# Optimization experiments

Hardware: AMD Instinct MI355X
Metric: run time of the kernel (lower is better)

The kernel has to match this reference:

```python
import jax, jax.numpy as jnp
from jax import lax
import numpy as np

V, T, K, R, H, EN, L = 10000, 100, 50, 300, 200, 800, 3
B = 128
TRAIN_SIZE = 100000
DELTA = 0.005


def setup_inputs():
    key = jax.random.key(0)
    ks = jax.random.split(key, 16)
    s = 0.02
    return {
        "bows": jax.random.uniform(ks[0], (B, V), jnp.float32) * 10.0 + 1e-3,
        "times": jax.random.randint(ks[1], (B,), 0, T),
        "rnn_inp": jax.random.uniform(ks[2], (T, V), jnp.float32),
        "rho_W": jax.random.normal(ks[3], (V, R), jnp.float32) * s,
        "mu_q_alpha": jax.random.normal(ks[4], (K, T, R), jnp.float32),
        "logsigma_q_alpha": jax.random.normal(ks[5], (K, T, R), jnp.float32) * 0.1 - 2.0,
        "qtheta_W1": jax.random.normal(ks[6], (EN, V + K), jnp.float32) * s,
        "qtheta_b1": jnp.zeros((EN,), jnp.float32),
        "qtheta_W2": jax.random.normal(ks[7], (EN, EN), jnp.float32) * s,
        "qtheta_b2": jnp.zeros((EN,), jnp.float32),
        "mu_theta_W": jax.random.normal(ks[8], (K, EN), jnp.float32) * s,
        "mu_theta_b": jnp.zeros((K,), jnp.float32),
        "ls_theta_W": jax.random.normal(ks[9], (K, EN), jnp.float32) * s,
        "ls_theta_b": jnp.zeros((K,), jnp.float32),
        "eta_map_W": jax.random.normal(ks[10], (H, V), jnp.float32) * s,
        "eta_map_b": jnp.zeros((H,), jnp.float32),
        "lstm_Wih": jax.random.normal(ks[11], (L, 4 * H, H), jnp.float32) * s,
        "lstm_Whh": jax.random.normal(ks[12], (L, 4 * H, H), jnp.float32) * s,
        "lstm_bih": jnp.zeros((L, 4 * H), jnp.float32),
        "lstm_bhh": jnp.zeros((L, 4 * H), jnp.float32),
        "mu_eta_W": jax.random.normal(ks[13], (K, H + K), jnp.float32) * s,
        "mu_eta_b": jnp.zeros((K,), jnp.float32),
        "ls_eta_W": jax.random.normal(ks[14], (K, H + K), jnp.float32) * s,
        "ls_eta_b": jnp.zeros((K,), jnp.float32),
    }


def _kl(q_mu, q_ls, p_mu, p_ls):
    # KL(N(q_mu, exp(q_ls)) || N(p_mu, exp(p_ls))), logsigma == log-variance as in torch code
    return 0.5 * jnp.sum((jnp.exp(q_ls) + (q_mu - p_mu) ** 2) / (jnp.exp(p_ls) + 1e-6) - 1.0 + p_ls - q_ls, axis=-1)


def _lstm(x, Wih, Whh, bih, bhh):
    # x: [T, H]; L stacked LSTM layers (batch of 1 squeezed), torch gate order i,f,g,o
    for l in range(Wih.shape[0]):
        Wi, Wh, bi, bh = Wih[l], Whh[l], bih[l], bhh[l]
        Hd = Wh.shape[1]

        def step(carry, xt, Wi=Wi, Wh=Wh, bi=bi, bh=bh):
            h, c = carry
            g = Wi @ xt + Wh @ h + bi + bh
            i, f, gg, o = jnp.split(g, 4)
            c = jax.nn.sigmoid(f) * c + jax.nn.sigmoid(i) * jnp.tanh(gg)
            h = jax.nn.sigmoid(o) * jnp.tanh(c)
            return (h, c), h

        z = jnp.zeros((Hd,), x.dtype)
        _, x = lax.scan(step, (z, z), x)
    return x


def _forward(bows, rnn_inp, rho_W, mu_q_alpha, logsigma_q_alpha, qtheta_W1, qtheta_b1, qtheta_W2, qtheta_b2, mu_theta_W, mu_theta_b, ls_theta_W, ls_theta_b, eta_map_W, eta_map_b, lstm_Wih, lstm_Whh, lstm_bih, lstm_bhh, mu_eta_W, mu_eta_b, ls_eta_W, ls_eta_b, times):
    log_delta = jnp.log(jnp.float32(DELTA))
    # --- eta: LSTM over word-freq sequence, then sequential mu/logsigma/KL per t ---
    out = _lstm(rnn_inp @ eta_map_W.T + eta_map_b, lstm_Wih, lstm_Whh, lstm_bih, lstm_bhh)  # [T,H]
    p_ls_seq = jnp.concatenate([jnp.zeros((1,), jnp.float32), jnp.full((T - 1,), log_delta, jnp.float32)])

    def eta_step(eta_prev, xs):
        o_t, p_ls = xs
        x = jnp.concatenate([o_t, eta_prev])
        mu = mu_eta_W @ x + mu_eta_b
        ls = ls_eta_W @ x + ls_eta_b
        kl = _kl(mu, ls, eta_prev, jnp.full_like(mu, p_ls))
        return mu, (mu, kl)  # eval-mode reparameterize -> eta_t = mu

    _, (etas, kls) = lax.scan(eta_step, jnp.zeros((K,), jnp.float32), (out, p_ls_seq))
    kl_eta = kls.sum()
    # --- theta encoder ---
    nb = bows / bows.sum(1, keepdims=True)
    eta_td = etas[times]  # [B,K]
    h = jax.nn.relu(jnp.concatenate([nb, eta_td], axis=1) @ qtheta_W1.T + qtheta_b1)
    h = jax.nn.relu(h @ qtheta_W2.T + qtheta_b2)
    mu_t = h @ mu_theta_W.T + mu_theta_b
    ls_t = h @ ls_theta_W.T + ls_theta_b
    theta = jax.nn.softmax(mu_t, axis=-1)  # z = mu (eval-mode reparam)
    coeff = jnp.float32(TRAIN_SIZE / bows.shape[0])
    kl_theta = _kl(mu_t, ls_t, eta_td, jnp.zeros_like(mu_t)).sum() * coeff
    # --- alpha: with eval-mode reparam, alphas == mu, so KL is fully vectorized ---
    muT = jnp.transpose(mu_q_alpha, (1, 0, 2))  # [T,K,R]
    lsT = jnp.transpose(logsigma_q_alpha, (1, 0, 2))
    alphas = muT
    p_mu = jnp.concatenate([jnp.zeros((1, K, R), muT.dtype), alphas[:-1]], axis=0)
    p_ls = jnp.concatenate([jnp.zeros((1, K, R), muT.dtype), jnp.full((T - 1, K, R), log_delta, muT.dtype)], axis=0)
    kl_alpha = _kl(muT, lsT, p_mu, p_ls).sum()
    # --- beta and NLL ---
    logit = alphas.reshape(T * K, R) @ rho_W.T  # [T*K, V]
    beta = jax.nn.softmax(logit, axis=-1).reshape(T, K, V)
    beta_d = beta[times]  # [B,K,V]
    loglik = jnp.log(jnp.einsum('bk,bkv->bv', theta, beta_d) + 1e-12)
    nll = (-(loglik * bows).sum(-1)).sum() * coeff
    loss = nll + kl_eta + kl_theta + kl_alpha
    return loss, nll, kl_eta, kl_theta, kl_alpha


def reference(bows, times, rnn_inp, rho_W, mu_q_alpha, logsigma_q_alpha, qtheta_W1, qtheta_b1, qtheta_W2, qtheta_b2, mu_theta_W, mu_theta_b, ls_theta_W, ls_theta_b, eta_map_W, eta_map_b, lstm_Wih, lstm_Whh, lstm_bih, lstm_bhh, mu_eta_W, mu_eta_b, ls_eta_W, ls_eta_b):
    return _forward(bows, rnn_inp, rho_W, mu_q_alpha, logsigma_q_alpha, qtheta_W1, qtheta_b1, qtheta_W2, qtheta_b2, mu_theta_W, mu_theta_b, ls_theta_W, ls_theta_b, eta_map_W, eta_map_b, lstm_Wih, lstm_Whh, lstm_bih, lstm_bhh, mu_eta_W, mu_eta_b, ls_eta_W, ls_eta_b, times)
```

## Files before the change

kernel.cpp:

```cpp
#include <hip/hip_runtime.h>


typedef unsigned int u32;
typedef unsigned short u16;
typedef _Float16 f16;
typedef f16 f16x2 __attribute__((ext_vector_type(2)));
typedef short bf16x8 __attribute__((ext_vector_type(8)));
typedef float f32x4 __attribute__((ext_vector_type(4)));
typedef u32 u32x4 __attribute__((ext_vector_type(4)));

#define LOG_DELTA (-5.2983174f)
#define COEFF 781.25f

#if defined(__has_builtin)
#if __has_builtin(__builtin_amdgcn_sdot4)
#define HAVE_SDOT4 1
#endif
#endif

__device__ __forceinline__ float bf2f(u16 a) { return __uint_as_float(((u32)a) << 16); }
__device__ __forceinline__ u16 f2bf(float f) {
  u32 u = __float_as_uint(f);
  u32 r = (u + 0x7fffu + ((u >> 16) & 1u)) >> 16;
  return (u16)r;
}
__device__ __forceinline__ float fdot2(u32 w, u32 h, float acc) {
  return __builtin_amdgcn_fdot2(__builtin_bit_cast(f16x2, w), __builtin_bit_cast(f16x2, h), acc, false);
}
__device__ __forceinline__ int dot4i8(u32 a, u32 b, int c) {
#ifdef HAVE_SDOT4
  return __builtin_amdgcn_sdot4(a, b, c, false);
#else
  int s = c;
  s += ((int)(a << 24) >> 24) * ((int)(b << 24) >> 24);
  s += ((int)(a << 16) >> 24) * ((int)(b << 16) >> 24);
  s += ((int)(a << 8) >> 24) * ((int)(b << 8) >> 24);
  s += ((int)a >> 24) * ((int)b >> 24);
  return s;
#endif
}
__device__ __forceinline__ float sigm(float x) { return 1.f / (1.f + __expf(-x)); }
__device__ __forceinline__ float ftanh(float x) { float t = __expf(2.f * x); return (t - 1.f) / (t + 1.f); }
__device__ __forceinline__ u16 f2h(float x) { return __builtin_bit_cast(u16, (f16)x); }
__device__ __forceinline__ float h2f(u16 x) { return (float)__builtin_bit_cast(f16, x); }
__device__ __forceinline__ void async_load16(const u16* g, u16* l) {
  __builtin_amdgcn_global_load_lds((const __attribute__((address_space(1))) u32*)g,
                                   (__attribute__((address_space(3))) u32*)l, 16, 0, 0);
}


__global__ __launch_bounds__(64) void k_zero(float* __restrict__ accum) {
  if (threadIdx.x < 8) accum[threadIdx.x] = 0.f;
}

__global__ __launch_bounds__(256) void k_nb(const float* __restrict__ bows, float* __restrict__ nb) {
  __shared__ float red[256];
  const int b = blockIdx.x, tid = threadIdx.x;
  float s = 0.f;
  for (int v = tid; v < 10000; v += 256) s += bows[b * 10000 + v];
  red[tid] = s; __syncthreads();
  for (int o = 128; o > 0; o >>= 1) { if (tid < o) red[tid] += red[tid + o]; __syncthreads(); }
  const float inv = 1.f / red[0];
  for (int v = tid; v < 10000; v += 256) nb[b * 10000 + v] = bows[b * 10000 + v] * inv;
}

__global__ __launch_bounds__(256) void k_bsum(const float* __restrict__ a, const float* __restrict__ b,
                                              float* __restrict__ o, int n) {
  int i = blockIdx.x * 256 + threadIdx.x;
  if (i < n) o[i] = a[i] + b[i];
}

__global__ __launch_bounds__(256) void k_fill(float* __restrict__ C, const float* __restrict__ bias,
                                              int N, int total) {
  for (int i = blockIdx.x * 256 + threadIdx.x; i < total; i += gridDim.x * 256)
    C[i] = bias[i % N];
}

__global__ __launch_bounds__(256) void k_relu(float* __restrict__ C, int total) {
  for (int i = blockIdx.x * 256 + threadIdx.x; i < total; i += gridDim.x * 256) {
    float v = C[i];
    C[i] = v > 0.f ? v : 0.f;
  }
}

__global__ __launch_bounds__(128) void k_stack2(const float* __restrict__ a, const float* __restrict__ b,
                                                float* __restrict__ o) {
  const int t = threadIdx.x;
  if (t < 50) o[t] = a[t];
  else if (t < 100) o[t] = b[t - 50];
}

__global__ __launch_bounds__(64) void k_quant_whh(const float* __restrict__ Whh,
                                                  u32* __restrict__ whq, float* __restrict__ rowscale) {
  const int gr = blockIdx.x;
  const int lane = threadIdx.x;
  __shared__ float wrow[200];
  const float* src = Whh + (size_t)gr * 200;
  float m = 0.f;
  for (int c = lane; c < 200; c += 64) { float v = src[c]; wrow[c] = v; m = fmaxf(m, fabsf(v)); }
  for (int o = 32; o > 0; o >>= 1) m = fmaxf(m, __shfl_down(m, o));
  m = __shfl(m, 0);
  const float qs = (m > 0.f) ? 127.f / m : 0.f;
  __syncthreads();
  const int l = gr / 800, rr = gr - l * 800;
  if (lane < 52) {
    u32 d = 0;
    if (lane < 50) {
#pragma unroll
      for (int b = 0; b < 4; ++b) {
        int q = __float2int_rn(wrow[lane * 4 + b] * qs);
        q = max(-127, min(127, q));
        d |= ((u32)(q & 0xff)) << (8 * b);
      }
    }
    whq[l * 41600 + rr * 52 + lane] = d;
  }
  if (lane == 0) rowscale[gr] = (m > 0.f) ? m / 127.f : 0.f;
}

__global__ __launch_bounds__(256) void k_cvt_eta(const float* __restrict__ muW, const float* __restrict__ lsW,
                                                 u16* __restrict__ out) {
  int idx = blockIdx.x * 256 + threadIdx.x;
  if (idx >= 25000) return;
  int r = idx / 250, c = idx - r * 250;
  float v = (r < 50) ? muW[r * 250 + c] : lsW[(r - 50) * 250 + c];
  out[idx] = f2h(v);
}

__global__ __launch_bounds__(256) void k_prep_A(const float* __restrict__ muq, u16* __restrict__ Abf) {
  int idx = blockIdx.x * 256 + threadIdx.x;
  if (idx >= 5120 * 320) return;
  int r = idx % 320, m = idx / 320;
  float v = 0.f;
  if (r < 300 && m < 5000) { int t = m / 50, k = m - t * 50; v = muq[k * 30000 + t * 300 + r]; }
  Abf[idx] = f2bf(v);
}
__global__ __launch_bounds__(256) void k_prep_B(const float* __restrict__ rho, u16* __restrict__ Bbf) {
  int idx = blockIdx.x * 256 + threadIdx.x;
  if (idx >= 10112 * 320) return;
  int r = idx % 320, n = idx / 320;
  float v = (r < 300 && n < 10000) ? rho[n * 300 + r] : 0.f;
  Bbf[idx] = f2bf(v);
}


#define ST 64
#define SBK 32

template<int AMODE, int BMODE, int EPI>
__global__ __launch_bounds__(256) void gemm64(
    const float* __restrict__ A, const float* __restrict__ Bm, const float* __restrict__ Bm2,
    const float* __restrict__ bias, float* __restrict__ C,
    int M, int N, int Kd, int lda, int ldb,
    const int* __restrict__ times, const float* __restrict__ etas)
{
  __shared__ __align__(16) float As[SBK][ST + 4];
  __shared__ __align__(16) float Bs[SBK][ST + 4];
  const int tid = threadIdx.x;
  const int tx = tid & 15, ty = tid >> 4;
  const int m_base = blockIdx.x * ST, n_base = blockIdx.y * ST;
  float acc[4][4] = {};
  const int nkt = (Kd + SBK - 1) / SBK;
  const int per = (nkt + gridDim.z - 1) / gridDim.z;
  const int kt0 = blockIdx.z * per;
  const int kt1 = min(nkt, kt0 + per);
  const int lkk = tid & 31;
  const int lrow = tid >> 5;
  for (int kt = kt0; kt < kt1; ++kt) {
    const int kg = kt * SBK + lkk;
#pragma unroll
    for (int i = 0; i < 8; ++i) {
      const int m = m_base + lrow + i * 8;
      float v = 0.f;
      if (m < M && kg < Kd) {
        if (AMODE == 0) v = A[(size_t)m * lda + kg];
        else {
          if (kg < 10000) v = A[(size_t)m * 10000 + kg];
          else v = etas[times[m] * 50 + (kg - 10000)];
        }
      }
      As[lkk][lrow + i * 8] = v;
    }
#pragma unroll
    for (int i = 0; i < 8; ++i) {
      const int n = n_base + lrow + i * 8;
      float v = 0.f;
      if (n < N && kg < Kd) {
        if (BMODE == 0) v = Bm[(size_t)n * ldb + kg];
        else v = (n < 50) ? Bm[(size_t)n * ldb + kg] : Bm2[(size_t)(n - 50) * ldb + kg];
      }
      Bs[lkk][lrow + i * 8] = v;
    }
    __syncthreads();
#pragma unroll
    for (int kk = 0; kk < SBK; ++kk) {
      const float4 a4 = *(const float4*)&As[kk][ty * 4];
      const float4 b4 = *(const float4*)&Bs[kk][tx * 4];
      const float av[4] = {a4.x, a4.y, a4.z, a4.w};
      const float bv[4] = {b4.x, b4.y, b4.z, b4.w};
#pragma unroll
      for (int i = 0; i < 4; ++i)
#pragma unroll
        for (int j = 0; j < 4; ++j) acc[i][j] += av[i] * bv[j];
    }
    __syncthreads();
  }
#pragma unroll
  for (int i = 0; i < 4; ++i) {
    const int m = m_base + ty * 4 + i;
    if (m >= M) continue;
#pragma unroll
    for (int j = 0; j < 4; ++j) {
      const int n = n_base + tx * 4 + j;
      if (n >= N) continue;
      float v = acc[i][j];
      if (EPI == 1) { C[(size_t)m * N + n] = v + bias[n]; }
      else if (EPI == 2) { v += bias[n]; C[(size_t)m * N + n] = v > 0.f ? v : 0.f; }
      else if (EPI == 5) { atomicAdd(&C[(size_t)m * N + n], v); }
      else { C[(size_t)m * N + n] = v; }
    }
  }
}


__global__ __launch_bounds__(256) void gemm_mfma_bT(
    const u16* __restrict__ A, const u16* __restrict__ B, u16* __restrict__ C,
    int M, int N)
{
  __shared__ u16 As[128 * 32];
  __shared__ u16 Bs[128 * 32];
  const int tid = threadIdx.x;
  const int l = tid & 63, w = tid >> 6;
  const int wm = w & 1, wn = w >> 1;
  const int m0 = blockIdx.x * 128, n0 = blockIdx.y * 128;
  f32x4 acc[4][4] = {};
  const int arow = l >> 2;
  const int acol = (l & 3) * 8;
  for (int kt = 0; kt < 10; ++kt) {
    const int k0 = kt * 32;
#pragma unroll
    for (int c = 0; c < 2; ++c) {
      const int i = w + c * 4;
      async_load16(A + (size_t)(m0 + i * 16 + arow) * 320 + k0 + acol, As + i * 512);
      async_load16(B + (size_t)(n0 + i * 16 + arow) * 320 + k0 + acol, Bs + i * 512);
    }
    __syncthreads();
    bf16x8 af[4], bfr[4];
#pragma unroll
    for (int x = 0; x < 4; ++x) {
      af[x]  = *(const bf16x8*)&As[(wm * 64 + x * 16 + (l & 15)) * 32 + (l >> 4) * 8];
      bfr[x] = *(const bf16x8*)&Bs[(wn * 64 + x * 16 + (l & 15)) * 32 + (l >> 4) * 8];
    }
#pragma unroll
    for (int x = 0; x < 4; ++x)
#pragma unroll
      for (int y = 0; y < 4; ++y)
        acc[x][y] = __builtin_amdgcn_mfma_f32_16x16x32_bf16(af[x], bfr[y], acc[x][y], 0, 0, 0);
    __syncthreads();
  }
  const int col = l & 15, quad = l >> 4;
#pragma unroll
  for (int x = 0; x < 4; ++x) {
    const int gmB = m0 + wm * 64 + x * 16 + quad * 4;
#pragma unroll
    for (int y = 0; y < 4; ++y) {
      const int gn = n0 + wn * 64 + y * 16 + col;
      if (gn >= N) continue;
#pragma unroll
      for (int r = 0; r < 4; ++r) {
        const int gm = gmB + r;
        if (gm < M) C[(size_t)gm * N + gn] = f2bf(acc[x][y][r]);
      }
    }
  }
}


__global__ __launch_bounds__(512, 1) void lstm_scan_reg(
    const u32* __restrict__ whq,
    const float* __restrict__ rowscale,
    const float* __restrict__ xproj,
    float* __restrict__ hseq,
    u16* __restrict__ hseq16,
    const int write16)
{
  __shared__ u16 pg[800];
  __shared__ __align__(16) u32 hq[52];
  __shared__ float wmax[8];
  __shared__ float hscale_s[1];
  const int tid = threadIdx.x;
  const int act = (tid < 400);
  const int r0 = tid, r1 = tid + 400;
  u32x4 wA4[13], wB4[13];
  float rsA = 0.f, rsB = 0.f;
  float xpA = 0.f, xpB = 0.f;
  if (act) {
    const u32x4* gA = (const u32x4*)(whq + (size_t)r0 * 52);
    const u32x4* gB = (const u32x4*)(whq + (size_t)r1 * 52);
#pragma unroll
    for (int i = 0; i < 13; ++i) { wA4[i] = gA[i]; wB4[i] = gB[i]; }
    rsA = rowscale[r0]; rsB = rowscale[r1];
    xpA = xproj[r0]; xpB = xproj[r1];
  }
  if (tid < 52) hq[tid] = 0;
  if (tid < 8) wmax[tid] = 0.f;
  if (tid == 0) hscale_s[0] = 0.f;
  float c_reg = 0.f;
  __syncthreads();
  for (int t = 0; t < 100; ++t) {
    if (act) {
      float nxA = 0.f, nxB = 0.f;
      if (t < 99) { nxA = xproj[(t + 1) * 800 + r0]; nxB = xproj[(t + 1) * 800 + r1]; }
      const float hdq = hscale_s[0];
      u32x4 hv4[13];
#pragma unroll
      for (int i = 0; i < 13; ++i) hv4[i] = *((const u32x4*)hq + i);
      int aA = 0, aB = 0;
#pragma unroll
      for (int g = 0; g < 50; ++g) {
        const u32 h = hv4[g >> 2][g & 3];
        aA = dot4i8(wA4[g >> 2][g & 3], h, aA);
        aB = dot4i8(wB4[g >> 2][g & 3], h, aB);
      }
      pg[r0] = f2h((float)aA * (rsA * hdq) + xpA);
      pg[r1] = f2h((float)aB * (rsB * hdq) + xpB);
      xpA = nxA; xpB = nxB;
    }
    __syncthreads();
    float hv = 0.f;
    if (tid < 200) {
      float gi = sigm(h2f(pg[tid]));
      float gf = sigm(h2f(pg[200 + tid]));
      float gg = ftanh(h2f(pg[400 + tid]));
      float go = sigm(h2f(pg[600 + tid]));
      c_reg = gf * c_reg + gi * gg;
      hv = go * ftanh(c_reg);
      hseq[t * 200 + tid] = hv;
      if (write16) hseq16[t * 200 + tid] = f2h(hv);
    }
    float m = fabsf(hv);
    for (int o = 32; o > 0; o >>= 1) m = fmaxf(m, __shfl_down(m, o));
    if ((tid & 63) == 0) wmax[tid >> 6] = m;
    __syncthreads();
    if (tid < 200) {
      const float hm = fmaxf(fmaxf(wmax[0], wmax[1]), fmaxf(wmax[2], wmax[3]));
      const float qs = (hm > 0.f) ? 127.f / hm : 0.f;
      int q = __float2int_rn(hv * qs);
      q = max(-127, min(127, q));
      ((signed char*)hq)[tid] = (signed char)q;
      if (tid == 0) hscale_s[0] = (hm > 0.f) ? hm / 127.f : 0.f;
    }
    __syncthreads();
  }
}


__global__ __launch_bounds__(512) void eta_scan(
    const u16* __restrict__ etaWh,
    const float* __restrict__ mub, const float* __restrict__ lsb,
    const u16* __restrict__ hseq16,
    float* __restrict__ etas, float* __restrict__ accum)
{
  __shared__ __align__(4) u16 EW[25000];
  __shared__ __align__(4) u16 HS[20000];
  __shared__ __align__(4) u16 xh[252];
  __shared__ float pc[400];
  __shared__ float mu_ls[100];
  __shared__ float bias[100];
  __shared__ float eta_f[52];
  const int tid = threadIdx.x;
  for (int i = tid; i < 12500; i += 512) ((u32*)EW)[i] = ((const u32*)etaWh)[i];
  for (int i = tid; i < 10000; i += 512) ((u32*)HS)[i] = ((const u32*)hseq16)[i];
  if (tid < 100) bias[tid] = (tid < 50) ? mub[tid] : lsb[tid - 50];
  if (tid < 52) eta_f[tid] = 0.f;
  if (tid < 252) xh[tid] = 0;
  float klacc = 0.f;
  const int r = tid % 100, s4 = tid / 100;
  const int q0 = s4 * 32, q1 = min(125, q0 + 32);
  __syncthreads();
  for (int t = 0; t < 100; ++t) {
    if (tid < 100) ((u32*)xh)[tid] = ((const u32*)HS)[t * 100 + tid];
    __syncthreads();
    if (tid < 400) {
      float acc = 0.f;
      const u32* Wr = (const u32*)EW;
      const u32* X2 = (const u32*)xh;
      for (int q = q0; q < q1; ++q) acc = fdot2(Wr[r * 125 + q], X2[q], acc);
      pc[s4 * 100 + r] = acc;
    }
    __syncthreads();
    if (tid < 100)
      mu_ls[tid] = pc[tid] + pc[100 + tid] + pc[200 + tid] + pc[300 + tid] + bias[tid];
    __syncthreads();
    if (tid < 50) {
      float mu = mu_ls[tid], ls = mu_ls[50 + tid], ep = eta_f[tid];
      float pls = (t == 0) ? 0.f : LOG_DELTA;
      float pv = __expf(pls) + 1e-6f;
      float d = mu - ep;
      klacc += 0.5f * ((__expf(ls) + d * d) / pv - 1.f + pls - ls);
      etas[t * 50 + tid] = mu;
      eta_f[tid] = mu;
      xh[200 + tid] = f2h(mu);
    }
    __syncthreads();
  }
  if (tid < 64) {
    for (int o = 32; o > 0; o >>= 1) klacc += __shfl_down(klacc, o);
    if (tid == 0) accum[0] = klacc;
  }
}


__global__ __launch_bounds__(64) void k_theta(const float* __restrict__ mul,
                                              const float* __restrict__ etas, const int* __restrict__ times,
                                              float* __restrict__ theta, float* __restrict__ accum) {
  const int b = blockIdx.x, lane = threadIdx.x;
  float m_ = 0.f, l_ = 0.f, e_ = 0.f, mx = -1e30f;
  if (lane < 50) {
    m_ = mul[b * 100 + lane];
    l_ = mul[b * 100 + 50 + lane];
    e_ = etas[times[b] * 50 + lane];
    mx = m_;
  }
  for (int o = 32; o > 0; o >>= 1) mx = fmaxf(mx, __shfl_down(mx, o));
  mx = __shfl(mx, 0);
  float ex = (lane < 50) ? __expf(m_ - mx) : 0.f;
  float sum = ex;
  for (int o = 32; o > 0; o >>= 1) sum += __shfl_down(sum, o);
  sum = __shfl(sum, 0);
  if (lane < 50) theta[b * 50 + lane] = ex / sum;
  float kl = 0.f;
  if (lane < 50) {
    float d = m_ - e_;
    kl = 0.5f * ((__expf(l_) + d * d) / (1.f + 1e-6f) - 1.f - l_);
  }
  for (int o = 32; o > 0; o >>= 1) kl += __shfl_down(kl, o);
  if (lane == 0) atomicAdd(accum + 1, kl);
}


__global__ __launch_bounds__(256) void k_rowsum(const u16* __restrict__ logit, float* __restrict__ Z) {
  const int r = blockIdx.x, tid = threadIdx.x;
  const u32* row = (const u32*)(logit + (size_t)r * 10000);
  __shared__ float red[256];
  float s = 0.f;
  for (int v = tid; v < 5000; v += 256) {
    u32 p = row[v];
    s += __expf(bf2f((u16)(p & 0xffffu))) + __expf(bf2f((u16)(p >> 16)));
  }
  red[tid] = s; __syncthreads();
  for (int o = 128; o > 0; o >>= 1) { if (tid < o) red[tid] += red[tid + o]; __syncthreads(); }
  if (tid == 0) Z[r] = red[0];
}


__global__ __launch_bounds__(256) void k_nll(const u16* __restrict__ logit, const float* __restrict__ Z,
                                             const float* __restrict__ theta, const float* __restrict__ bows,
                                             const int* __restrict__ times, float* __restrict__ accum) {
  const int b = blockIdx.x, seg = blockIdx.y, tid = threadIdx.x;
  const int t = times[b];
  __shared__ float c2[52];
  __shared__ float red[256];
  if (tid < 50) c2[tid] = theta[b * 50 + tid] / Z[t * 50 + tid];
  __syncthreads();
  float part = 0.f;
  const int v0 = seg * 1250, v1 = v0 + 1250;
  const u16* base = logit + (size_t)t * 500000;
  for (int v = v0 + tid; v < v1; v += 256) {
    float ssv = 1e-12f;
#pragma unroll
    for (int k = 0; k < 50; ++k) ssv += c2[k] * __expf(bf2f(base[k * 10000 + v]));
    part += bows[b * 10000 + v] * __logf(ssv);
  }
  red[tid] = part; __syncthreads();
  for (int o = 128; o > 0; o >>= 1) { if (tid < o) red[tid] += red[tid + o]; __syncthreads(); }
  if (tid == 0) atomicAdd(accum + 3, -red[0]);
}


__global__ __launch_bounds__(256) void k_alpha_kl(const float* __restrict__ muq, const float* __restrict__ lsq,
                                                  float* __restrict__ accum) {
  __shared__ float red[256];
  const int tid = threadIdx.x;
  float s = 0.f;
  for (int i = blockIdx.x * 256 + tid; i < 1500000; i += gridDim.x * 256) {
    int r = i % 300;
    int tk = i / 300;
    int k = tk % 50;
    int t = tk / 50;
    size_t idx = (size_t)k * 30000 + (size_t)t * 300 + r;
    float mu = muq[idx], ls = lsq[idx];
    float pm = 0.f, pls = 0.f;
    if (t > 0) { pm = muq[idx - 300]; pls = LOG_DELTA; }
    float d = mu - pm;
    s += 0.5f * ((__expf(ls) + d * d) / (__expf(pls) + 1e-6f) - 1.f + pls - ls);
  }
  red[tid] = s; __syncthreads();
  for (int o = 128; o > 0; o >>= 1) { if (tid < o) red[tid] += red[tid + o]; __syncthreads(); }
  if (tid == 0) atomicAdd(accum + 2, red[0]);
}


__global__ __launch_bounds__(64) void k_final(const float* __restrict__ accum, float* __restrict__ out) {
  if (threadIdx.x == 0) {
    float nll = accum[3] * COEFF;
    float kl_eta = accum[0];
    float kl_theta = accum[1] * COEFF;
    float kl_alpha = accum[2];
    out[0] = nll + kl_eta + kl_theta + kl_alpha;
    out[1] = nll;
    out[2] = kl_eta;
    out[3] = kl_theta;
    out[4] = kl_alpha;
  }
}


extern "C" void kernel_launch(void* const* d_in, const int* in_sizes, int n_in,
                              void* d_out, int out_size, void* d_ws, size_t ws_size,
                              hipStream_t stream) {
  (void)in_sizes; (void)n_in; (void)out_size; (void)ws_size;
  const float* bows   = (const float*)d_in[0];
  const int*   times  = (const int*)d_in[1];
  const float* rnn_in = (const float*)d_in[2];
  const float* rho_W  = (const float*)d_in[3];
  const float* muq    = (const float*)d_in[4];
  const float* lsq    = (const float*)d_in[5];
  const float* qW1    = (const float*)d_in[6];
  const float* qb1    = (const float*)d_in[7];
  const float* qW2    = (const float*)d_in[8];
  const float* qb2    = (const float*)d_in[9];
  const float* muthW  = (const float*)d_in[10];
  const float* muthb  = (const float*)d_in[11];
  const float* lsthW  = (const float*)d_in[12];
  const float* lsthb  = (const float*)d_in[13];
  const float* emW    = (const float*)d_in[14];
  const float* emb    = (const float*)d_in[15];
  const float* Wih    = (const float*)d_in[16];
  const float* Whh    = (const float*)d_in[17];
  const float* bih    = (const float*)d_in[18];
  const float* bhh    = (const float*)d_in[19];
  const float* mueW   = (const float*)d_in[20];
  const float* mueb   = (const float*)d_in[21];
  const float* lseW   = (const float*)d_in[22];
  const float* lseb   = (const float*)d_in[23];
  float* out = (float*)d_out;
  float* ws = (float*)d_ws;

  float* accum = ws + 0;
  float* nb    = ws + 8;
  float* x0    = ws + 1280008;
  float* xproj = ws + 1300008;
  float* hsA   = ws + 1380008;
  float* hsB   = ws + 1400008;
  u32*   whq   = (u32*)(ws + 1420008);
  float* rowsc = ws + 1544808;
  float* bias2 = ws + 1547208;
  u16*   etaWh = (u16*)(ws + 1547408);
  float* hsC   = ws + 1560008;
  u16*   hs16  = (u16*)(ws + 1580008);
  float* bsum  = ws + 1660008;
  float* etas  = ws + 1662408;
  float* h1    = ws + 1667408;
  float* h2    = ws + 1769808;
  float* mul   = ws + 1872208;
  float* theta = ws + 1885008;
  float* Zrow  = ws + 1891408;
  u16*   A_bf  = (u16*)(ws + 1896408);
  u16*   B_bf  = (u16*)(ws + 2715608);
  u16*   logit = (u16*)(ws + 4333528);

  k_zero<<<1, 64, 0, stream>>>(accum);
  k_nb<<<128, 256, 0, stream>>>(bows, nb);
  k_quant_whh<<<2400, 64, 0, stream>>>(Whh, whq, rowsc);
  k_bsum<<<10, 256, 0, stream>>>(bih, bhh, bsum, 2400);
  k_cvt_eta<<<98, 256, 0, stream>>>(mueW, lseW, etaWh);
  k_prep_A<<<6400, 256, 0, stream>>>(muq, A_bf);
  k_prep_B<<<12640, 256, 0, stream>>>(rho_W, B_bf);
  k_stack2<<<1, 128, 0, stream>>>(muthb, lsthb, bias2);

  k_fill<<<79, 256, 0, stream>>>(x0, emb, 200, 20000);
  gemm64<0, 0, 5><<<dim3(2, 4, 32), 256, 0, stream>>>(rnn_in, emW, nullptr, nullptr, x0,
                                                      100, 200, 10000, 10000, 10000, nullptr, nullptr);

  const float* lin[3] = {x0, hsA, hsB};
  float* lout[3] = {hsA, hsB, hsC};
  for (int l = 0; l < 3; ++l) {
    gemm64<0, 0, 1><<<dim3(2, 13, 1), 256, 0, stream>>>(lin[l], Wih + l * 160000, nullptr,
                                                        bsum + l * 800, xproj,
                                                        100, 800, 200, 200, 200, nullptr, nullptr);
    lstm_scan_reg<<<1, 512, 0, stream>>>(whq + l * 41600, rowsc + l * 800, xproj,
                                         lout[l], hs16, (l == 2) ? 1 : 0);
  }
  eta_scan<<<1, 512, 0, stream>>>(etaWh, mueb, lseb, hs16, etas, accum);

  k_fill<<<400, 256, 0, stream>>>(h1, qb1, 800, 102400);
  gemm64<2, 0, 5><<<dim3(2, 13, 24), 256, 0, stream>>>(nb, qW1, nullptr, nullptr, h1,
                                                       128, 800, 10050, 10000, 10050, times, etas);
  k_relu<<<400, 256, 0, stream>>>(h1, 102400);
  k_fill<<<400, 256, 0, stream>>>(h2, qb2, 800, 102400);
  gemm64<0, 0, 5><<<dim3(2, 13, 4), 256, 0, stream>>>(h1, qW2, nullptr, nullptr, h2,
                                                      128, 800, 800, 800, 800, nullptr, nullptr);
  k_relu<<<400, 256, 0, stream>>>(h2, 102400);
  k_fill<<<50, 256, 0, stream>>>(mul, bias2, 100, 12800);
  gemm64<0, 1, 5><<<dim3(2, 2, 5), 256, 0, stream>>>(h2, muthW, lsthW, nullptr, mul,
                                                     128, 100, 800, 800, 800, nullptr, nullptr);
  k_theta<<<128, 64, 0, stream>>>(mul, etas, times, theta, accum);

  gemm_mfma_bT<<<dim3(40, 79), 256, 0, stream>>>(A_bf, B_bf, logit, 5000, 10000);
  k_rowsum<<<5000, 256, 0, stream>>>(logit, Zrow);
  k_nll<<<dim3(128, 8), 256, 0, stream>>>(logit, Zrow, theta, bows, times, accum);

  k_alpha_kl<<<512, 256, 0, stream>>>(muq, lsq, accum);
  k_final<<<1, 64, 0, stream>>>(accum, out);
}
```

Baseline: 1.260 ms.

## Hoist eta input projection into parallel GEMM and shrink recurrent eta scan

The eta recurrence previously computed the full 250-wide dot product, LSTM hidden state plus previous eta, at every timestep inside a single 512-thread block. This change precomputes the hidden-state part for all 100 timesteps with a batched GEMM plus bias, then runs a 64-thread scan that keeps only the 50x50 eta-to-eta weights in fp32 registers. The aim is to shorten the serial critical path and drop the fp16 conversion and shared-memory staging. It adds a GEMM launch and two small setup kernels, and changes precision from fp16 dot products to fp32.

```diff
diff --git a/kernel.cpp b/kernel.cpp
--- a/kernel.cpp
+++ b/kernel.cpp
@@ -23,9 +23,6 @@
   u32 u = __float_as_uint(f);
   u32 r = (u + 0x7fffu + ((u >> 16) & 1u)) >> 16;
   return (u16)r;
-}
-__device__ __forceinline__ float fdot2(u32 w, u32 h, float acc) {
-  return __builtin_amdgcn_fdot2(__builtin_bit_cast(f16x2, w), __builtin_bit_cast(f16x2, h), acc, false);
 }
 __device__ __forceinline__ int dot4i8(u32 a, u32 b, int c) {
 #ifdef HAVE_SDOT4
@@ -116,15 +113,6 @@
     whq[l * 41600 + rr * 52 + lane] = d;
   }
   if (lane == 0) rowscale[gr] = (m > 0.f) ? m / 127.f : 0.f;
-}
-
-__global__ __launch_bounds__(256) void k_cvt_eta(const float* __restrict__ muW, const float* __restrict__ lsW,
-                                                 u16* __restrict__ out) {
-  int idx = blockIdx.x * 256 + threadIdx.x;
-  if (idx >= 25000) return;
-  int r = idx / 250, c = idx - r * 250;
-  float v = (r < 50) ? muW[r * 250 + c] : lsW[(r - 50) * 250 + c];
-  out[idx] = f2h(v);
 }
 
 __global__ __launch_bounds__(256) void k_prep_A(const float* __restrict__ muq, u16* __restrict__ Abf) {
@@ -280,9 +268,7 @@
     const u32* __restrict__ whq,
     const float* __restrict__ rowscale,
     const float* __restrict__ xproj,
-    float* __restrict__ hseq,
-    u16* __restrict__ hseq16,
-    const int write16)
+    float* __restrict__ hseq)
 {
   __shared__ u16 pg[800];
   __shared__ __align__(16) u32 hq[52];
@@ -336,7 +322,6 @@
       c_reg = gf * c_reg + gi * gg;
       hv = go * ftanh(c_reg);
       hseq[t * 200 + tid] = hv;
-      if (write16) hseq16[t * 200 + tid] = f2h(hv);
     }
     float m = fabsf(hv);
     for (int o = 32; o > 0; o >>= 1) m = fmaxf(m, __shfl_down(m, o));
@@ -355,59 +340,65 @@
 }
 
 
-__global__ __launch_bounds__(512) void eta_scan(
-    const u16* __restrict__ etaWh,
-    const float* __restrict__ mub, const float* __restrict__ lsb,
-    const u16* __restrict__ hseq16,
+__global__ __launch_bounds__(64, 1) void eta_scan_reg(
+    const float* __restrict__ muW, const float* __restrict__ lsW,
+    const float* __restrict__ pc0,
     float* __restrict__ etas, float* __restrict__ accum)
 {
-  __shared__ __align__(4) u16 EW[25000];
-  __shared__ __align__(4) u16 HS[20000];
-  __shared__ __align__(4) u16 xh[252];
-  __shared__ float pc[400];
-  __shared__ float mu_ls[100];
-  __shared__ float bias[100];
-  __shared__ float eta_f[52];
-  const int tid = threadIdx.x;
-  for (int i = tid; i < 12500; i += 512) ((u32*)EW)[i] = ((const u32*)etaWh)[i];
-  for (int i = tid; i < 10000; i += 512) ((u32*)HS)[i] = ((const u32*)hseq16)[i];
-  if (tid < 100) bias[tid] = (tid < 50) ? mub[tid] : lsb[tid - 50];
-  if (tid < 52) eta_f[tid] = 0.f;
-  if (tid < 252) xh[tid] = 0;
+  __shared__ __align__(16) float ep[52];
+  const int j = threadIdx.x;
+  const int act = (j < 50);
+  float wmu[52], wls[52];
+  if (act) {
+#pragma unroll
+    for (int k = 0; k < 25; ++k) {
+      float2 a = *(const float2*)(muW + (size_t)j * 250 + 200 + 2 * k);
+      float2 b = *(const float2*)(lsW + (size_t)j * 250 + 200 + 2 * k);
+      wmu[2 * k] = a.x; wmu[2 * k + 1] = a.y;
+      wls[2 * k] = b.x; wls[2 * k + 1] = b.y;
+    }
+    wmu[50] = wmu[51] = wls[50] = wls[51] = 0.f;
+  } else {
+#pragma unroll
+    for (int k = 0; k < 52; ++k) { wmu[k] = 0.f; wls[k] = 0.f; }
+  }
+  if (j < 52) ep[j] = 0.f;
   float klacc = 0.f;
-  const int r = tid % 100, s4 = tid / 100;
-  const int q0 = s4 * 32, q1 = min(125, q0 + 32);
+  float mye = 0.f;
+  float pmu = act ? pc0[j] : 0.f;
+  float pls_ = act ? pc0[50 + j] : 0.f;
   __syncthreads();
   for (int t = 0; t < 100; ++t) {
-    if (tid < 100) ((u32*)xh)[tid] = ((const u32*)HS)[t * 100 + tid];
-    __syncthreads();
-    if (tid < 400) {
-      float acc = 0.f;
-      const u32* Wr = (const u32*)EW;
-      const u32* X2 = (const u32*)xh;
-      for (int q = q0; q < q1; ++q) acc = fdot2(Wr[r * 125 + q], X2[q], acc);
-      pc[s4 * 100 + r] = acc;
-    }
-    __syncthreads();
-    if (tid < 100)
-      mu_ls[tid] = pc[tid] + pc[100 + tid] + pc[200 + tid] + pc[300 + tid] + bias[tid];
-    __syncthreads();
-    if (tid < 50) {
-      float mu = mu_ls[tid], ls = mu_ls[50 + tid], ep = eta_f[tid];
-      float pls = (t == 0) ? 0.f : LOG_DELTA;
-      float pv = __expf(pls) + 1e-6f;
-      float d = mu - ep;
+    float nmu = 0.f, nls = 0.f;
+    if (act && t < 99) { nmu = pc0[(t + 1) * 100 + j]; nls = pc0[(t + 1) * 100 + 50 + j]; }
+    float ma[4] = {pmu, 0.f, 0.f, 0.f};
+    float la[4] = {pls_, 0.f, 0.f, 0.f};
+    const float4* e4 = (const float4*)ep;
+#pragma unroll
+    for (int i = 0; i < 13; ++i) {
+      const float4 e = e4[i];
+      ma[0] += wmu[4 * i + 0] * e.x; ma[1] += wmu[4 * i + 1] * e.y;
+      ma[2] += wmu[4 * i + 2] * e.z; ma[3] += wmu[4 * i + 3] * e.w;
+      la[0] += wls[4 * i + 0] * e.x; la[1] += wls[4 * i + 1] * e.y;
+      la[2] += wls[4 * i + 2] * e.z; la[3] += wls[4 * i + 3] * e.w;
+    }
+    const float mu = (ma[0] + ma[1]) + (ma[2] + ma[3]);
+    const float ls = (la[0] + la[1]) + (la[2] + la[3]);
+    __syncthreads();
+    if (act) {
+      const float pls = (t == 0) ? 0.f : LOG_DELTA;
+      const float pv = __expf(pls) + 1e-6f;
+      const float d = mu - mye;
       klacc += 0.5f * ((__expf(ls) + d * d) / pv - 1.f + pls - ls);
-      etas[t * 50 + tid] = mu;
-      eta_f[tid] = mu;
-      xh[200 + tid] = f2h(mu);
-    }
-    __syncthreads();
-  }
-  if (tid < 64) {
-    for (int o = 32; o > 0; o >>= 1) klacc += __shfl_down(klacc, o);
-    if (tid == 0) accum[0] = klacc;
-  }
+      etas[t * 50 + j] = mu;
+      mye = mu;
+      ep[j] = mu;
+    }
+    __syncthreads();
+    pmu = nmu; pls_ = nls;
+  }
+  for (int o = 32; o > 0; o >>= 1) klacc += __shfl_down(klacc, o);
+  if (j == 0) accum[0] = klacc;
 }
 
 
@@ -556,9 +547,9 @@
   u32*   whq   = (u32*)(ws + 1420008);
   float* rowsc = ws + 1544808;
   float* bias2 = ws + 1547208;
-  u16*   etaWh = (u16*)(ws + 1547408);
+  float* pc0   = ws + 1547408;
+  float* bias2e= ws + 1558008;
   float* hsC   = ws + 1560008;
-  u16*   hs16  = (u16*)(ws + 1580008);
   float* bsum  = ws + 1660008;
   float* etas  = ws + 1662408;
   float* h1    = ws + 1667408;
@@ -574,10 +565,11 @@
   k_nb<<<128, 256, 0, stream>>>(bows, nb);
   k_quant_whh<<<2400, 64, 0, stream>>>(Whh, whq, rowsc);
   k_bsum<<<10, 256, 0, stream>>>(bih, bhh, bsum, 2400);
-  k_cvt_eta<<<98, 256, 0, stream>>>(mueW, lseW, etaWh);
   k_prep_A<<<6400, 256, 0, stream>>>(muq, A_bf);
   k_prep_B<<<12640, 256, 0, stream>>>(rho_W, B_bf);
   k_stack2<<<1, 128, 0, stream>>>(muthb, lsthb, bias2);
+  k_stack2<<<1, 128, 0, stream>>>(mueb, lseb, bias2e);
+  k_fill<<<40, 256, 0, stream>>>(pc0, bias2e, 100, 10000);
 
   k_fill<<<79, 256, 0, stream>>>(x0, emb, 200, 20000);
   gemm64<0, 0, 5><<<dim3(2, 4, 32), 256, 0, stream>>>(rnn_in, emW, nullptr, nullptr, x0,
@@ -589,10 +581,11 @@
     gemm64<0, 0, 1><<<dim3(2, 13, 1), 256, 0, stream>>>(lin[l], Wih + l * 160000, nullptr,
                                                         bsum + l * 800, xproj,
                                                         100, 800, 200, 200, 200, nullptr, nullptr);
-    lstm_scan_reg<<<1, 512, 0, stream>>>(whq + l * 41600, rowsc + l * 800, xproj,
-                                         lout[l], hs16, (l == 2) ? 1 : 0);
-  }
-  eta_scan<<<1, 512, 0, stream>>>(etaWh, mueb, lseb, hs16, etas, accum);
+    lstm_scan_reg<<<1, 512, 0, stream>>>(whq + l * 41600, rowsc + l * 800, xproj, lout[l]);
+  }
+  gemm64<0, 1, 5><<<dim3(2, 2, 7), 256, 0, stream>>>(hsC, mueW, lseW, nullptr, pc0,
+                                                     100, 100, 200, 200, 250, nullptr, nullptr);
+  eta_scan_reg<<<1, 64, 0, stream>>>(mueW, lseW, pc0, etas, accum);
 
   k_fill<<<400, 256, 0, stream>>>(h1, qb1, 800, 102400);
   gemm64<2, 0, 5><<<dim3(2, 13, 24), 256, 0, stream>>>(nb, qW1, nullptr, nullptr, h1,
```

Result: faster. 1.153 ms (-8.5%).
